# Kernel optimization log

Measured on AMD Instinct MI355X. Metric: run time of the kernel, lower is better.

Reference implementation:

```python
import jax, jax.numpy as jnp
import numpy as np

NUM_EXPERTS = 64
HIDDEN = 1024
INTER = 768
N_TOKENS = 32768


def setup_inputs() -> dict:
    key = jax.random.key(0)
    k1, k2, k3, k4 = jax.random.split(key, 4)
    init_std = 0.02
    return {
        "hidden_states": jax.random.normal(k1, (N_TOKENS, HIDDEN), dtype=jnp.float32),
        "gate_proj": jax.random.normal(k2, (NUM_EXPERTS, INTER, HIDDEN), dtype=jnp.float32) * init_std,
        "up_proj": jax.random.normal(k3, (NUM_EXPERTS, INTER, HIDDEN), dtype=jnp.float32) * init_std,
        "down_proj": jax.random.normal(k4, (NUM_EXPERTS, HIDDEN, INTER), dtype=jnp.float32) * init_std,
        "expert_idx": 3,
    }


def reference(hidden_states, gate_proj, up_proj, down_proj, expert_idx):
    # gather this expert's weights: [INTER, HIDDEN] / [HIDDEN, INTER]
    g = gate_proj[expert_idx]
    u = up_proj[expert_idx]
    d = down_proj[expert_idx]
    gate_out = hidden_states @ g.T                      # [N, INTER]
    up_out = hidden_states @ u.T                        # [N, INTER]
    h = jax.nn.silu(gate_out) * up_out                  # SiLU(gate) * up
    return h @ d.T                                      # [N, HIDDEN]
```

## Files before the change

### kernel.cpp

```cpp
#include <hip/hip_runtime.h>


typedef __bf16 bf16;
typedef bf16 bf16x8 __attribute__((ext_vector_type(8)));
typedef bf16 bf16x4 __attribute__((ext_vector_type(4)));
typedef float f32x4 __attribute__((ext_vector_type(4)));

static constexpr int M_TOK  = 32768;
static constexpr int HIDDEN = 1024;
static constexpr int INTER  = 768;

#define BM 128
#define BN 128
#define BNG 64
#define BK 32


__global__ __launch_bounds__(256) void cast_h_kernel(const float* __restrict__ in,
                                                     bf16* __restrict__ out) {
    int i = blockIdx.x * 256 + threadIdx.x;
    f32x4 v = ((const f32x4*)in)[i];
    bf16x4 o;
    o.x = (bf16)v.x; o.y = (bf16)v.y; o.z = (bf16)v.z; o.w = (bf16)v.w;
    ((bf16x4*)out)[i] = o;
}

__global__ __launch_bounds__(256) void cast_w_kernel(const float* __restrict__ G,
                                                     const float* __restrict__ U,
                                                     const float* __restrict__ D,
                                                     const int* __restrict__ eidx,
                                                     bf16* __restrict__ Gb,
                                                     bf16* __restrict__ Ub,
                                                     bf16* __restrict__ Db) {
    const int e = *eidx;
    const int EW4 = (INTER * HIDDEN) / 4;
    int i = blockIdx.x * 256 + threadIdx.x;
    if (i >= 3 * EW4) return;
    int which = i / EW4;
    int r = i - which * EW4;
    const float* src = (which == 0) ? G : (which == 1) ? U : D;
    bf16* dst = (which == 0) ? Gb : (which == 1) ? Ub : Db;
    f32x4 v = ((const f32x4*)(src + (size_t)e * (INTER * HIDDEN)))[r];
    bf16x4 o;
    o.x = (bf16)v.x; o.y = (bf16)v.y; o.z = (bf16)v.z; o.w = (bf16)v.w;
    ((bf16x4*)dst)[r] = o;
}


__global__ __launch_bounds__(256, 2) void gemm_gateup(const bf16* __restrict__ A,
                                                      const bf16* __restrict__ G,
                                                      const bf16* __restrict__ U,
                                                      bf16* __restrict__ Hout) {
    const int K = HIDDEN;
    const int N = INTER;
    __shared__ bf16 sA[BM * BK];
    __shared__ bf16 sG[BNG * BK];
    __shared__ bf16 sU[BNG * BK];

    const int t    = threadIdx.x;
    const int wave = t >> 6;
    const int lane = t & 63;
    const int wr   = wave >> 1;
    const int wc   = wave & 1;
    const int m0   = blockIdx.x * BM;
    const int n0   = blockIdx.y * BNG;

    const int srow = wave * 16 + (lane >> 2);
    const int scol = (lane & 3) * 8;
    const int ldsOff = wave * 512 + lane * 8;

    f32x4 accg[4][2];
    f32x4 accu[4][2];
#pragma unroll
    for (int i = 0; i < 4; i++)
#pragma unroll
        for (int j = 0; j < 2; j++) {
            accg[i][j] = (f32x4){0.f, 0.f, 0.f, 0.f};
            accu[i][j] = (f32x4){0.f, 0.f, 0.f, 0.f};
        }

    const bf16* pA = A + (size_t)(m0 + srow) * K + scol;
    const bf16* pG = G + (size_t)(n0 + srow) * K + scol;
    const bf16* pU = U + (size_t)(n0 + srow) * K + scol;

    for (int kt = 0; kt < K; kt += BK) {
#pragma unroll
        for (int j = 0; j < 2; ++j) {
            __builtin_amdgcn_global_load_lds(
                (const __attribute__((address_space(1))) void*)(pA + (size_t)j * 64 * K + kt),
                (__attribute__((address_space(3))) void*)(sA + j * 2048 + ldsOff), 16, 0, 0);
        }
        __builtin_amdgcn_global_load_lds(
            (const __attribute__((address_space(1))) void*)(pG + kt),
            (__attribute__((address_space(3))) void*)(sG + ldsOff), 16, 0, 0);
        __builtin_amdgcn_global_load_lds(
            (const __attribute__((address_space(1))) void*)(pU + kt),
            (__attribute__((address_space(3))) void*)(sU + ldsOff), 16, 0, 0);
        __syncthreads();

        bf16x8 af[4], gf[2], uf[2];
        const int fk = (lane >> 4) * 8;
        const int fr = lane & 15;
#pragma unroll
        for (int i = 0; i < 4; i++)
            af[i] = *(const bf16x8*)(sA + (wr * 64 + i * 16 + fr) * BK + fk);
#pragma unroll
        for (int j = 0; j < 2; j++) {
            gf[j] = *(const bf16x8*)(sG + (wc * 32 + j * 16 + fr) * BK + fk);
            uf[j] = *(const bf16x8*)(sU + (wc * 32 + j * 16 + fr) * BK + fk);
        }
#pragma unroll
        for (int i = 0; i < 4; i++)
#pragma unroll
            for (int j = 0; j < 2; j++) {
                accg[i][j] = __builtin_amdgcn_mfma_f32_16x16x32_bf16(af[i], gf[j], accg[i][j], 0, 0, 0);
                accu[i][j] = __builtin_amdgcn_mfma_f32_16x16x32_bf16(af[i], uf[j], accu[i][j], 0, 0, 0);
            }
        __syncthreads();
    }

    const int crow = (lane >> 4) * 4;
    const int ccol = lane & 15;
#pragma unroll
    for (int i = 0; i < 4; i++)
#pragma unroll
        for (int j = 0; j < 2; j++) {
            int col = n0 + wc * 32 + j * 16 + ccol;
#pragma unroll
            for (int r = 0; r < 4; r++) {
                int row = m0 + wr * 64 + i * 16 + crow + r;
                float g = accg[i][j][r];
                float u = accu[i][j][r];
                float s = g / (1.0f + __expf(-g));
                Hout[(size_t)row * N + col] = (bf16)(s * u);
            }
        }
}


__global__ __launch_bounds__(256, 2) void gemm_down(const bf16* __restrict__ A,
                                                    const bf16* __restrict__ B,
                                                    float* __restrict__ Out) {
    const int K = INTER;
    const int N = HIDDEN;
    __shared__ bf16 sA[BM * BK];
    __shared__ bf16 sB[BM * BK];

    const int t    = threadIdx.x;
    const int wave = t >> 6;
    const int lane = t & 63;
    const int wr   = wave >> 1;
    const int wc   = wave & 1;
    const int m0   = blockIdx.x * BM;
    const int n0   = blockIdx.y * BN;

    const int srow = wave * 16 + (lane >> 2);
    const int scol = (lane & 3) * 8;
    const int ldsOff = wave * 512 + lane * 8;

    f32x4 acc[4][4];
#pragma unroll
    for (int i = 0; i < 4; i++)
#pragma unroll
        for (int j = 0; j < 4; j++)
            acc[i][j] = (f32x4){0.f, 0.f, 0.f, 0.f};

    const bf16* pA = A + (size_t)(m0 + srow) * K + scol;
    const bf16* pB = B + (size_t)(n0 + srow) * K + scol;

    for (int kt = 0; kt < K; kt += BK) {
#pragma unroll
        for (int j = 0; j < 2; ++j) {
            __builtin_amdgcn_global_load_lds(
                (const __attribute__((address_space(1))) void*)(pA + (size_t)j * 64 * K + kt),
                (__attribute__((address_space(3))) void*)(sA + j * 2048 + ldsOff), 16, 0, 0);
            __builtin_amdgcn_global_load_lds(
                (const __attribute__((address_space(1))) void*)(pB + (size_t)j * 64 * K + kt),
                (__attribute__((address_space(3))) void*)(sB + j * 2048 + ldsOff), 16, 0, 0);
        }
        __syncthreads();

        bf16x8 af[4], bfg[4];
        const int fk = (lane >> 4) * 8;
        const int fr = lane & 15;
#pragma unroll
        for (int i = 0; i < 4; i++) {
            af[i]  = *(const bf16x8*)(sA + (wr * 64 + i * 16 + fr) * BK + fk);
            bfg[i] = *(const bf16x8*)(sB + (wc * 64 + i * 16 + fr) * BK + fk);
        }
#pragma unroll
        for (int i = 0; i < 4; i++)
#pragma unroll
            for (int j = 0; j < 4; j++)
                acc[i][j] = __builtin_amdgcn_mfma_f32_16x16x32_bf16(af[i], bfg[j], acc[i][j], 0, 0, 0);
        __syncthreads();
    }

    const int crow = (lane >> 4) * 4;
    const int ccol = lane & 15;
#pragma unroll
    for (int i = 0; i < 4; i++)
#pragma unroll
        for (int j = 0; j < 4; j++) {
            int col = n0 + wc * 64 + j * 16 + ccol;
#pragma unroll
            for (int r = 0; r < 4; r++) {
                int row = m0 + wr * 64 + i * 16 + crow + r;
                Out[(size_t)row * N + col] = acc[i][j][r];
            }
        }
}


extern "C" void kernel_launch(void* const* d_in, const int* in_sizes, int n_in,
                              void* d_out, int out_size, void* d_ws, size_t ws_size,
                              hipStream_t stream) {
    const float* H = (const float*)d_in[0];
    const float* G = (const float*)d_in[1];
    const float* U = (const float*)d_in[2];
    const float* D = (const float*)d_in[3];
    const int* eidx = (const int*)d_in[4];
    float* out = (float*)d_out;

    char* ws = (char*)d_ws;
    bf16* Hb = (bf16*)(ws);
    bf16* Gb = (bf16*)(ws + 67108864);
    bf16* Ub = (bf16*)(ws + 67108864 + 1 * 1572864);
    bf16* Db = (bf16*)(ws + 67108864 + 2 * 1572864);
    bf16* hb = (bf16*)(ws + 67108864 + 3 * 1572864);

    cast_h_kernel<<<32768, 256, 0, stream>>>(H, Hb);
    cast_w_kernel<<<2304, 256, 0, stream>>>(G, U, D, eidx, Gb, Ub, Db);
    dim3 g1(M_TOK / BM, INTER / BNG);
    gemm_gateup<<<g1, 256, 0, stream>>>(Hb, Gb, Ub, hb);
    dim3 g2(M_TOK / BM, HIDDEN / BN);
    gemm_down<<<g2, 256, 0, stream>>>(hb, Db, out);
}
```

Before: 676.4 us.

## Double-buffer LDS tiles in both GEMMs, swap grid order, fuse cast kernels

Both GEMM kernels now keep two LDS buffers, so the next K-tile's global-to-LDS loads are issued before the MFMAs on the current tile run. This hides load latency behind compute and removes one barrier per iteration. The grid axes are swapped so consecutive blocks share the same activation row tile, which should improve L2 reuse of A. The two cast kernels are merged into a single launch. Doubling the shared memory per block may lower occupancy.

```diff
diff --git a/kernel.cpp b/kernel.cpp
--- a/kernel.cpp
+++ b/kernel.cpp
@@ -16,34 +16,36 @@
 #define BK 32
 
 
-__global__ __launch_bounds__(256) void cast_h_kernel(const float* __restrict__ in,
-                                                     bf16* __restrict__ out) {
-    int i = blockIdx.x * 256 + threadIdx.x;
-    f32x4 v = ((const f32x4*)in)[i];
-    bf16x4 o;
-    o.x = (bf16)v.x; o.y = (bf16)v.y; o.z = (bf16)v.z; o.w = (bf16)v.w;
-    ((bf16x4*)out)[i] = o;
-}
-
-__global__ __launch_bounds__(256) void cast_w_kernel(const float* __restrict__ G,
-                                                     const float* __restrict__ U,
-                                                     const float* __restrict__ D,
-                                                     const int* __restrict__ eidx,
-                                                     bf16* __restrict__ Gb,
-                                                     bf16* __restrict__ Ub,
-                                                     bf16* __restrict__ Db) {
-    const int e = *eidx;
-    const int EW4 = (INTER * HIDDEN) / 4;
-    int i = blockIdx.x * 256 + threadIdx.x;
-    if (i >= 3 * EW4) return;
-    int which = i / EW4;
-    int r = i - which * EW4;
-    const float* src = (which == 0) ? G : (which == 1) ? U : D;
-    bf16* dst = (which == 0) ? Gb : (which == 1) ? Ub : Db;
-    f32x4 v = ((const f32x4*)(src + (size_t)e * (INTER * HIDDEN)))[r];
-    bf16x4 o;
-    o.x = (bf16)v.x; o.y = (bf16)v.y; o.z = (bf16)v.z; o.w = (bf16)v.w;
-    ((bf16x4*)dst)[r] = o;
+__global__ __launch_bounds__(256) void cast_all_kernel(const float* __restrict__ H,
+                                                       const float* __restrict__ G,
+                                                       const float* __restrict__ U,
+                                                       const float* __restrict__ D,
+                                                       const int* __restrict__ eidx,
+                                                       bf16* __restrict__ Hb,
+                                                       bf16* __restrict__ Gb,
+                                                       bf16* __restrict__ Ub,
+                                                       bf16* __restrict__ Db) {
+    const int b = blockIdx.x;
+    if (b < 32768) {
+        int i = b * 256 + threadIdx.x;
+        f32x4 v = ((const f32x4*)H)[i];
+        bf16x4 o;
+        o.x = (bf16)v.x; o.y = (bf16)v.y; o.z = (bf16)v.z; o.w = (bf16)v.w;
+        ((bf16x4*)Hb)[i] = o;
+    } else {
+        const int e = *eidx;
+        const int EW4 = (INTER * HIDDEN) / 4;
+        int i = (b - 32768) * 256 + threadIdx.x;
+        if (i >= 3 * EW4) return;
+        int which = i / EW4;
+        int r = i - which * EW4;
+        const float* src = (which == 0) ? G : (which == 1) ? U : D;
+        bf16* dst = (which == 0) ? Gb : (which == 1) ? Ub : Db;
+        f32x4 v = ((const f32x4*)(src + (size_t)e * (INTER * HIDDEN)))[r];
+        bf16x4 o;
+        o.x = (bf16)v.x; o.y = (bf16)v.y; o.z = (bf16)v.z; o.w = (bf16)v.w;
+        ((bf16x4*)dst)[r] = o;
+    }
 }
 
 
@@ -53,17 +55,17 @@
                                                       bf16* __restrict__ Hout) {
     const int K = HIDDEN;
     const int N = INTER;
-    __shared__ bf16 sA[BM * BK];
-    __shared__ bf16 sG[BNG * BK];
-    __shared__ bf16 sU[BNG * BK];
+    __shared__ bf16 sA[2][BM * BK];
+    __shared__ bf16 sG[2][BNG * BK];
+    __shared__ bf16 sU[2][BNG * BK];
 
     const int t    = threadIdx.x;
     const int wave = t >> 6;
     const int lane = t & 63;
     const int wr   = wave >> 1;
     const int wc   = wave & 1;
-    const int m0   = blockIdx.x * BM;
-    const int n0   = blockIdx.y * BNG;
+    const int n0   = blockIdx.x * BNG;
+    const int m0   = blockIdx.y * BM;
 
     const int srow = wave * 16 + (lane >> 2);
     const int scol = (lane & 3) * 8;
@@ -83,31 +85,39 @@
     const bf16* pG = G + (size_t)(n0 + srow) * K + scol;
     const bf16* pU = U + (size_t)(n0 + srow) * K + scol;
 
+#define STAGE_GU(bi, kk)                                                               \
+    do {                                                                               \
+        _Pragma("unroll")                                                              \
+        for (int j = 0; j < 2; ++j)                                                    \
+            __builtin_amdgcn_global_load_lds(                                          \
+                (const __attribute__((address_space(1))) void*)(pA + (size_t)j * 64 * K + (kk)), \
+                (__attribute__((address_space(3))) void*)(&sA[bi][0] + j * 2048 + ldsOff), 16, 0, 0); \
+        __builtin_amdgcn_global_load_lds(                                              \
+            (const __attribute__((address_space(1))) void*)(pG + (kk)),                \
+            (__attribute__((address_space(3))) void*)(&sG[bi][0] + ldsOff), 16, 0, 0); \
+        __builtin_amdgcn_global_load_lds(                                              \
+            (const __attribute__((address_space(1))) void*)(pU + (kk)),                \
+            (__attribute__((address_space(3))) void*)(&sU[bi][0] + ldsOff), 16, 0, 0); \
+    } while (0)
+
+    STAGE_GU(0, 0);
+    __syncthreads();
+
+    const int fk = (lane >> 4) * 8;
+    const int fr = lane & 15;
+    int cur = 0;
+
     for (int kt = 0; kt < K; kt += BK) {
-#pragma unroll
-        for (int j = 0; j < 2; ++j) {
-            __builtin_amdgcn_global_load_lds(
-                (const __attribute__((address_space(1))) void*)(pA + (size_t)j * 64 * K + kt),
-                (__attribute__((address_space(3))) void*)(sA + j * 2048 + ldsOff), 16, 0, 0);
-        }
-        __builtin_amdgcn_global_load_lds(
-            (const __attribute__((address_space(1))) void*)(pG + kt),
-            (__attribute__((address_space(3))) void*)(sG + ldsOff), 16, 0, 0);
-        __builtin_amdgcn_global_load_lds(
-            (const __attribute__((address_space(1))) void*)(pU + kt),
-            (__attribute__((address_space(3))) void*)(sU + ldsOff), 16, 0, 0);
-        __syncthreads();
+        if (kt + BK < K) STAGE_GU(cur ^ 1, kt + BK);
 
         bf16x8 af[4], gf[2], uf[2];
-        const int fk = (lane >> 4) * 8;
-        const int fr = lane & 15;
 #pragma unroll
         for (int i = 0; i < 4; i++)
-            af[i] = *(const bf16x8*)(sA + (wr * 64 + i * 16 + fr) * BK + fk);
+            af[i] = *(const bf16x8*)(&sA[cur][0] + (wr * 64 + i * 16 + fr) * BK + fk);
 #pragma unroll
         for (int j = 0; j < 2; j++) {
-            gf[j] = *(const bf16x8*)(sG + (wc * 32 + j * 16 + fr) * BK + fk);
-            uf[j] = *(const bf16x8*)(sU + (wc * 32 + j * 16 + fr) * BK + fk);
+            gf[j] = *(const bf16x8*)(&sG[cur][0] + (wc * 32 + j * 16 + fr) * BK + fk);
+            uf[j] = *(const bf16x8*)(&sU[cur][0] + (wc * 32 + j * 16 + fr) * BK + fk);
         }
 #pragma unroll
         for (int i = 0; i < 4; i++)
@@ -117,7 +127,9 @@
                 accu[i][j] = __builtin_amdgcn_mfma_f32_16x16x32_bf16(af[i], uf[j], accu[i][j], 0, 0, 0);
             }
         __syncthreads();
+        cur ^= 1;
     }
+#undef STAGE_GU
 
     const int crow = (lane >> 4) * 4;
     const int ccol = lane & 15;
@@ -143,16 +155,16 @@
                                                     float* __restrict__ Out) {
     const int K = INTER;
     const int N = HIDDEN;
-    __shared__ bf16 sA[BM * BK];
-    __shared__ bf16 sB[BM * BK];
+    __shared__ bf16 sA[2][BM * BK];
+    __shared__ bf16 sB[2][BM * BK];
 
     const int t    = threadIdx.x;
     const int wave = t >> 6;
     const int lane = t & 63;
     const int wr   = wave >> 1;
     const int wc   = wave & 1;
-    const int m0   = blockIdx.x * BM;
-    const int n0   = blockIdx.y * BN;
+    const int n0   = blockIdx.x * BN;
+    const int m0   = blockIdx.y * BM;
 
     const int srow = wave * 16 + (lane >> 2);
     const int scol = (lane & 3) * 8;
@@ -168,25 +180,34 @@
     const bf16* pA = A + (size_t)(m0 + srow) * K + scol;
     const bf16* pB = B + (size_t)(n0 + srow) * K + scol;
 
+#define STAGE_DN(bi, kk)                                                               \
+    do {                                                                               \
+        _Pragma("unroll")                                                              \
+        for (int j = 0; j < 2; ++j) {                                                  \
+            __builtin_amdgcn_global_load_lds(                                          \
+                (const __attribute__((address_space(1))) void*)(pA + (size_t)j * 64 * K + (kk)), \
+                (__attribute__((address_space(3))) void*)(&sA[bi][0] + j * 2048 + ldsOff), 16, 0, 0); \
+            __builtin_amdgcn_global_load_lds(                                          \
+                (const __attribute__((address_space(1))) void*)(pB + (size_t)j * 64 * K + (kk)), \
+                (__attribute__((address_space(3))) void*)(&sB[bi][0] + j * 2048 + ldsOff), 16, 0, 0); \
+        }                                                                              \
+    } while (0)
+
+    STAGE_DN(0, 0);
+    __syncthreads();
+
+    const int fk = (lane >> 4) * 8;
+    const int fr = lane & 15;
+    int cur = 0;
+
     for (int kt = 0; kt < K; kt += BK) {
-#pragma unroll
-        for (int j = 0; j < 2; ++j) {
-            __builtin_amdgcn_global_load_lds(
-                (const __attribute__((address_space(1))) void*)(pA + (size_t)j * 64 * K + kt),
-                (__attribute__((address_space(3))) void*)(sA + j * 2048 + ldsOff), 16, 0, 0);
-            __builtin_amdgcn_global_load_lds(
-                (const __attribute__((address_space(1))) void*)(pB + (size_t)j * 64 * K + kt),
-                (__attribute__((address_space(3))) void*)(sB + j * 2048 + ldsOff), 16, 0, 0);
-        }
-        __syncthreads();
+        if (kt + BK < K) STAGE_DN(cur ^ 1, kt + BK);
 
         bf16x8 af[4], bfg[4];
-        const int fk = (lane >> 4) * 8;
-        const int fr = lane & 15;
 #pragma unroll
         for (int i = 0; i < 4; i++) {
-            af[i]  = *(const bf16x8*)(sA + (wr * 64 + i * 16 + fr) * BK + fk);
-            bfg[i] = *(const bf16x8*)(sB + (wc * 64 + i * 16 + fr) * BK + fk);
+            af[i]  = *(const bf16x8*)(&sA[cur][0] + (wr * 64 + i * 16 + fr) * BK + fk);
+            bfg[i] = *(const bf16x8*)(&sB[cur][0] + (wc * 64 + i * 16 + fr) * BK + fk);
         }
 #pragma unroll
         for (int i = 0; i < 4; i++)
@@ -194,7 +215,9 @@
             for (int j = 0; j < 4; j++)
                 acc[i][j] = __builtin_amdgcn_mfma_f32_16x16x32_bf16(af[i], bfg[j], acc[i][j], 0, 0, 0);
         __syncthreads();
+        cur ^= 1;
     }
+#undef STAGE_DN
 
     const int crow = (lane >> 4) * 4;
     const int ccol = lane & 15;
@@ -229,10 +252,9 @@
     bf16* Db = (bf16*)(ws + 67108864 + 2 * 1572864);
     bf16* hb = (bf16*)(ws + 67108864 + 3 * 1572864);
 
-    cast_h_kernel<<<32768, 256, 0, stream>>>(H, Hb);
-    cast_w_kernel<<<2304, 256, 0, stream>>>(G, U, D, eidx, Gb, Ub, Db);
-    dim3 g1(M_TOK / BM, INTER / BNG);
+    cast_all_kernel<<<32768 + 2304, 256, 0, stream>>>(H, G, U, D, eidx, Hb, Gb, Ub, Db);
+    dim3 g1(INTER / BNG, M_TOK / BM);
     gemm_gateup<<<g1, 256, 0, stream>>>(Hb, Gb, Ub, hb);
-    dim3 g2(M_TOK / BM, HIDDEN / BN);
+    dim3 g2(HIDDEN / BN, M_TOK / BM);
     gemm_down<<<g2, 256, 0, stream>>>(hb, Db, out);
 }
```

Measured after the change: 679.6 us. About the same (+0.5%).
